# Performance work log

Hardware: AMD Instinct MI355X
Metric: run time of the kernel (lower is better)

## Reference

```python
import jax, jax.numpy as jnp
import numpy as np
from jax import lax

C = 64
EPS = 1e-6

def ln2d(x, w, b):
    # channel-wise LN over HxW per (n, c)
    mean = x.mean(axis=(2, 3), keepdims=True)
    var = ((x - mean) ** 2).mean(axis=(2, 3), keepdims=True)
    return (x - mean) / jnp.sqrt(var + EPS) * w + b

def pw(x, w, b):
    # 1x1 conv: w [O, I], b [O]
    return jnp.einsum('nihw,oi->nohw', x, w) + b[None, :, None, None]

def dwconv3(x, w, b):
    # depthwise 3x3, w [2C, 1, 3, 3]
    y = lax.conv_general_dilated(x, w, window_strides=(1, 1), padding='SAME',
                                 feature_group_count=x.shape[1],
                                 dimension_numbers=('NCHW', 'OIHW', 'NCHW'))
    return y + b[None, :, None, None]

def simple_gate(x):
    x1, x2 = jnp.split(x, 2, axis=1)
    return x1 * x2

def setup_inputs() -> dict:
    key = jax.random.key(0)
    ks = jax.random.split(key, 16)
    s = 0.05
    return {
        'x': jax.random.normal(ks[0], (8, C, 256, 256), jnp.float32),
        'ln1_w': jnp.ones((1, C, 1, 1), jnp.float32),
        'ln1_b': jnp.zeros((1, C, 1, 1), jnp.float32),
        'pw1_w': jax.random.normal(ks[1], (2 * C, C), jnp.float32) * s,
        'pw1_b': jnp.zeros((2 * C,), jnp.float32),
        'dw_w': jax.random.normal(ks[2], (2 * C, 1, 3, 3), jnp.float32) * s,
        'dw_b': jnp.zeros((2 * C,), jnp.float32),
        'sca_w': jax.random.normal(ks[3], (C, C), jnp.float32) * s,
        'sca_b': jnp.zeros((C,), jnp.float32),
        'pw2_w': jax.random.normal(ks[4], (C, C), jnp.float32) * s,
        'pw2_b': jnp.zeros((C,), jnp.float32),
        'ln2_w': jnp.ones((1, C, 1, 1), jnp.float32),
        'ln2_b': jnp.zeros((1, C, 1, 1), jnp.float32),
        'pw3_w': jax.random.normal(ks[5], (2 * C, C), jnp.float32) * s,
        'pw3_b': jnp.zeros((2 * C,), jnp.float32),
        'pw4_w': jax.random.normal(ks[6], (C, C), jnp.float32) * s,
        'pw4_b': jnp.zeros((C,), jnp.float32),
        'beta1': jax.random.normal(ks[7], (1, C, 1, 1), jnp.float32) * 0.1,
        'beta2': jax.random.normal(ks[8], (1, C, 1, 1), jnp.float32) * 0.1,
    }

def reference(x, ln1_w, ln1_b, pw1_w, pw1_b, dw_w, dw_b, sca_w, sca_b,
              pw2_w, pw2_b, ln2_w, ln2_b, pw3_w, pw3_b, pw4_w, pw4_b,
              beta1, beta2):
    y = ln2d(x, ln1_w, ln1_b)
    y = pw(y, pw1_w, pw1_b)
    y = dwconv3(y, dw_w, dw_b)
    y = simple_gate(y)
    # SCA: global avg pool -> 1x1 conv -> sigmoid scale
    s = y.mean(axis=(2, 3), keepdims=True)          # [N, C, 1, 1]
    w = jax.nn.sigmoid(pw(s, sca_w, sca_b))
    y = y * w
    y = pw(y, pw2_w, pw2_b)
    x = x + beta1 * y
    y2 = ln2d(x, ln2_w, ln2_b)
    y2 = pw(y2, pw3_w, pw3_b)
    y2 = simple_gate(y2)
    y2 = pw(y2, pw4_w, pw4_b)
    return x + beta2 * y2
```

## Files before the change

### kernel.cpp

```cpp
#include <hip/hip_runtime.h>
#include <hip/hip_bf16.h>

#define NB 8
#define CC 64
#define HWP 65536

typedef __attribute__((ext_vector_type(8))) short short8;
typedef __attribute__((ext_vector_type(4))) float f32x4;

__device__ __forceinline__ short f2bf(float f) {
  union { float f; unsigned u; } v; v.f = f;
  return (short)((v.u + 0x7FFF + ((v.u >> 16) & 1)) >> 16);
}
__device__ __forceinline__ float bf2f(unsigned short u) {
  union { unsigned u; float f; } v; v.u = ((unsigned)u) << 16; return v.f;
}

__global__ __launch_bounds__(256) void ln_stats_kernel(
    const float* __restrict__ x, const float* __restrict__ lw,
    const float* __restrict__ lb, float* __restrict__ a, float* __restrict__ b) {
  int plane = blockIdx.x;
  int c = plane & 63;
  const float4* p4 = (const float4*)(x + (size_t)plane * HWP);
  float s = 0.f, s2 = 0.f;
  for (int i = threadIdx.x; i < HWP / 4; i += 256) {
    float4 v = p4[i];
    s  += v.x + v.y + v.z + v.w;
    s2 += v.x * v.x + v.y * v.y + v.z * v.z + v.w * v.w;
  }
  for (int off = 32; off; off >>= 1) {
    s  += __shfl_down(s, off);
    s2 += __shfl_down(s2, off);
  }
  __shared__ float ls[4], ls2[4];
  int wid = threadIdx.x >> 6, lid = threadIdx.x & 63;
  if (lid == 0) { ls[wid] = s; ls2[wid] = s2; }
  __syncthreads();
  if (threadIdx.x == 0) {
    float S  = ls[0] + ls[1] + ls[2] + ls[3];
    float S2 = ls2[0] + ls2[1] + ls2[2] + ls2[3];
    float mean = S * (1.f / (float)HWP);
    float var  = S2 * (1.f / (float)HWP) - mean * mean;
    float rstd = rsqrtf(var + 1e-6f);
    float av = rstd * lw[c];
    a[plane] = av;
    b[plane] = lb[c] - mean * av;
  }
}

__global__ void fold_kernel(const float* __restrict__ w, const float* __restrict__ pb,
                            const float* __restrict__ a, const float* __restrict__ b,
                            float* __restrict__ wf, float* __restrict__ cf, int O) {
  int idx = blockIdx.x * blockDim.x + threadIdx.x;
  if (idx >= NB * O) return;
  int n = idx / O, o = idx - n * O;
  const float* an = a + n * 64;
  const float* bn = b + n * 64;
  const float* wo = w + o * 64;
  float* wfo = wf + (size_t)idx * 64;
  float cc = pb[o];
  for (int i = 0; i < 64; i++) { float wv = wo[i]; wfo[i] = wv * an[i]; cc += wv * bn[i]; }
  cf[idx] = cc;
}

__global__ __launch_bounds__(256, 2) void gemm_pw1_kernel(
    const float* __restrict__ x, const float* __restrict__ wf,
    const float* __restrict__ cf, unsigned short* __restrict__ z) {
  int n = blockIdx.y;
  int lane = threadIdx.x & 63, wid = threadIdx.x >> 6;
  int col = lane & 15, quad = lane >> 4;
  short8 a[8][2];
  const float* wfn = wf + (size_t)n * 128 * 64;
  #pragma unroll
  for (int mt = 0; mt < 8; mt++)
    #pragma unroll
    for (int ks = 0; ks < 2; ks++) {
      const float* wp = wfn + (mt * 16 + col) * 64 + ks * 32 + quad * 8;
      short8 v;
      #pragma unroll
      for (int j = 0; j < 8; j++) v[j] = f2bf(wp[j]);
      a[mt][ks] = v;
    }
  float cb[8][4];
  #pragma unroll
  for (int mt = 0; mt < 8; mt++)
    #pragma unroll
    for (int r = 0; r < 4; r++) cb[mt][r] = cf[n * 128 + mt * 16 + quad * 4 + r];
  const float* xn = x + (size_t)n * 64 * HWP;
  unsigned short* zn = z + (size_t)n * 128 * HWP;
  int pxbase = blockIdx.x * 512 + wid * 16 + col;
  for (int tile = 0; tile < 8; tile++) {
    int p = pxbase + tile * 64;
    short8 b[2];
    #pragma unroll
    for (int ks = 0; ks < 2; ks++)
      #pragma unroll
      for (int j = 0; j < 8; j++)
        b[ks][j] = f2bf(xn[(size_t)(ks * 32 + quad * 8 + j) * HWP + p]);
    f32x4 acc[8];
    #pragma unroll
    for (int mt = 0; mt < 8; mt++) {
      acc[mt] = (f32x4){0.f, 0.f, 0.f, 0.f};
      acc[mt] = __builtin_amdgcn_mfma_f32_16x16x32_bf16(a[mt][0], b[0], acc[mt], 0, 0, 0);
      acc[mt] = __builtin_amdgcn_mfma_f32_16x16x32_bf16(a[mt][1], b[1], acc[mt], 0, 0, 0);
    }
    #pragma unroll
    for (int mt = 0; mt < 8; mt++)
      #pragma unroll
      for (int r = 0; r < 4; r++)
        zn[(size_t)(mt * 16 + quad * 4 + r) * HWP + p] =
            (unsigned short)f2bf(acc[mt][r] + cb[mt][r]);
  }
}

__global__ __launch_bounds__(256) void dwgate_kernel(
    const unsigned short* __restrict__ z, const float* __restrict__ dww,
    const float* __restrict__ dwb, unsigned short* __restrict__ t,
    float* __restrict__ pooled2) {
  int blk = blockIdx.x;
  int plane = blk >> 1, half = blk & 1;
  int n = plane >> 6, c = plane & 63;
  int lane = threadIdx.x & 63, wv = threadIdx.x >> 6;
  const unsigned short* z0 = z + ((size_t)n * 128 + c) * HWP;
  const unsigned short* z1 = z0 + (size_t)64 * HWP;
  unsigned short* tp = t + (size_t)plane * HWP;
  float w0[9], w1[9];
  #pragma unroll
  for (int k = 0; k < 9; k++) { w0[k] = dww[c * 9 + k]; w1[k] = dww[(c + 64) * 9 + k]; }
  float bias0 = dwb[c], bias1 = dwb[c + 64];
  int r0 = half * 128 + wv * 32;
  int colb = lane * 4;

  float fa[3][4], la[3], ra[3];
  float fb[3][4], lb_[3], rb[3];

  auto loadrow = [&](const unsigned short* base, int h, float* f, float& l, float& r) {
    if ((unsigned)h < 256u) {
      ushort4 u = *(const ushort4*)(base + h * 256 + colb);
      f[0] = bf2f(u.x); f[1] = bf2f(u.y); f[2] = bf2f(u.z); f[3] = bf2f(u.w);
    } else {
      f[0] = f[1] = f[2] = f[3] = 0.f;
    }
    float ll = __shfl_up(f[3], 1);
    float rr = __shfl_down(f[0], 1);
    l = (lane == 0) ? 0.f : ll;
    r = (lane == 63) ? 0.f : rr;
  };

  loadrow(z0, r0 - 1, fa[0], la[0], ra[0]);
  loadrow(z1, r0 - 1, fb[0], lb_[0], rb[0]);
  loadrow(z0, r0,     fa[1], la[1], ra[1]);
  loadrow(z1, r0,     fb[1], lb_[1], rb[1]);

  float lsum = 0.f;
  #pragma unroll 2
  for (int h = r0; h < r0 + 32; h++) {
    loadrow(z0, h + 1, fa[2], la[2], ra[2]);
    loadrow(z1, h + 1, fb[2], lb_[2], rb[2]);
    float o0[4] = {bias0, bias0, bias0, bias0};
    float o1[4] = {bias1, bias1, bias1, bias1};
    #pragma unroll
    for (int rr_ = 0; rr_ < 3; rr_++) {
      float wl0 = w0[rr_ * 3], wc0 = w0[rr_ * 3 + 1], wr0 = w0[rr_ * 3 + 2];
      float wl1 = w1[rr_ * 3], wc1 = w1[rr_ * 3 + 1], wr1 = w1[rr_ * 3 + 2];
      const float* f0 = fa[rr_]; const float* f1 = fb[rr_];
      float l0 = la[rr_], r0h = ra[rr_], l1 = lb_[rr_], r1h = rb[rr_];
      o0[0] += wl0 * l0    + wc0 * f0[0] + wr0 * f0[1];
      o0[1] += wl0 * f0[0] + wc0 * f0[1] + wr0 * f0[2];
      o0[2] += wl0 * f0[1] + wc0 * f0[2] + wr0 * f0[3];
      o0[3] += wl0 * f0[2] + wc0 * f0[3] + wr0 * r0h;
      o1[0] += wl1 * l1    + wc1 * f1[0] + wr1 * f1[1];
      o1[1] += wl1 * f1[0] + wc1 * f1[1] + wr1 * f1[2];
      o1[2] += wl1 * f1[1] + wc1 * f1[2] + wr1 * f1[3];
      o1[3] += wl1 * f1[2] + wc1 * f1[3] + wr1 * r1h;
    }
    float g0 = o0[0] * o1[0], g1 = o0[1] * o1[1];
    float g2 = o0[2] * o1[2], g3 = o0[3] * o1[3];
    uint2 pk;
    pk.x = (unsigned)(unsigned short)f2bf(g0) | ((unsigned)(unsigned short)f2bf(g1) << 16);
    pk.y = (unsigned)(unsigned short)f2bf(g2) | ((unsigned)(unsigned short)f2bf(g3) << 16);
    *(uint2*)(tp + (size_t)h * 256 + colb) = pk;
    lsum += (g0 + g1) + (g2 + g3);
    #pragma unroll
    for (int i = 0; i < 4; i++) { fa[0][i] = fa[1][i]; fa[1][i] = fa[2][i];
                                  fb[0][i] = fb[1][i]; fb[1][i] = fb[2][i]; }
    la[0] = la[1]; la[1] = la[2]; ra[0] = ra[1]; ra[1] = ra[2];
    lb_[0] = lb_[1]; lb_[1] = lb_[2]; rb[0] = rb[1]; rb[1] = rb[2];
  }
  for (int off = 32; off; off >>= 1) lsum += __shfl_down(lsum, off);
  __shared__ float ls[4];
  if (lane == 0) ls[wv] = lsum;
  __syncthreads();
  if (threadIdx.x == 0) pooled2[plane * 2 + half] = ls[0] + ls[1] + ls[2] + ls[3];
}

__global__ void sca_kernel(const float* __restrict__ pooled2, const float* __restrict__ sw,
                           const float* __restrict__ sb, float* __restrict__ sca) {
  int idx = blockIdx.x * blockDim.x + threadIdx.x;
  if (idx >= 512) return;
  int n = idx >> 6, o = idx & 63;
  float s = sb[o];
  const float* pm = pooled2 + n * 64 * 2;
  for (int i = 0; i < 64; i++)
    s += sw[o * 64 + i] * (pm[i * 2] + pm[i * 2 + 1]) * (1.f / 65536.f);
  sca[idx] = 1.f / (1.f + expf(-s));
}

__global__ void fold_pw2_kernel(const float* __restrict__ w, const float* __restrict__ pb,
                                const float* __restrict__ sca, const float* __restrict__ beta1,
                                float* __restrict__ wf, float* __restrict__ cf) {
  int idx = blockIdx.x * blockDim.x + threadIdx.x;
  if (idx >= 512) return;
  int n = idx >> 6, o = idx & 6 * 10 + 3;
  o = idx & 63;
  float bt = beta1[o];
  const float* sn = sca + n * 64;
  float* wfo = wf + (size_t)idx * 64;
  for (int i = 0; i < 64; i++) wfo[i] = bt * w[o * 64 + i] * sn[i];
  cf[idx] = bt * pb[o];
}

__global__ __launch_bounds__(256, 2) void gemm_pw2_kernel(
    const unsigned short* __restrict__ t, const float* __restrict__ x,
    const float* __restrict__ wf, const float* __restrict__ cf,
    float* __restrict__ x1, float* __restrict__ part_sum, float* __restrict__ part_sq) {
  __shared__ float red_s[4][64], red_q[4][64];
  int n = blockIdx.y;
  int lane = threadIdx.x & 63, wid = threadIdx.x >> 6;
  int col = lane & 15, quad = lane >> 4;
  short8 a[4][2];
  const float* wfn = wf + (size_t)n * 64 * 64;
  #pragma unroll
  for (int mt = 0; mt < 4; mt++)
    #pragma unroll
    for (int ks = 0; ks < 2; ks++) {
      const float* wp = wfn + (mt * 16 + col) * 64 + ks * 32 + quad * 8;
      short8 v;
      #pragma unroll
      for (int j = 0; j < 8; j++) v[j] = f2bf(wp[j]);
      a[mt][ks] = v;
    }
  float cb[4][4];
  #pragma unroll
  for (int mt = 0; mt < 4; mt++)
    #pragma unroll
    for (int r = 0; r < 4; r++) cb[mt][r] = cf[n * 64 + mt * 16 + quad * 4 + r];
  const unsigned short* tn = t + (size_t)n * 64 * HWP;
  const float* xn = x + (size_t)n * 64 * HWP;
  float* x1n = x1 + (size_t)n * 64 * HWP;
  int pxbase = blockIdx.x * 512 + wid * 16 + col;
  float sacc[4][4], qacc[4][4];
  #pragma unroll
  for (int mt = 0; mt < 4; mt++)
    #pragma unroll
    for (int r = 0; r < 4; r++) { sacc[mt][r] = 0.f; qacc[mt][r] = 0.f; }
  for (int tile = 0; tile < 8; tile++) {
    int p = pxbase + tile * 64;
    short8 b[2];
    #pragma unroll
    for (int ks = 0; ks < 2; ks++)
      #pragma unroll
      for (int j = 0; j < 8; j++)
        b[ks][j] = (short)tn[(size_t)(ks * 32 + quad * 8 + j) * HWP + p];
    f32x4 acc[4];
    #pragma unroll
    for (int mt = 0; mt < 4; mt++) {
      acc[mt] = (f32x4){0.f, 0.f, 0.f, 0.f};
      acc[mt] = __builtin_amdgcn_mfma_f32_16x16x32_bf16(a[mt][0], b[0], acc[mt], 0, 0, 0);
      acc[mt] = __builtin_amdgcn_mfma_f32_16x16x32_bf16(a[mt][1], b[1], acc[mt], 0, 0, 0);
    }
    #pragma unroll
    for (int mt = 0; mt < 4; mt++)
      #pragma unroll
      for (int r = 0; r < 4; r++) {
        size_t idx = (size_t)(mt * 16 + quad * 4 + r) * HWP + p;
        float v = xn[idx] + acc[mt][r] + cb[mt][r];
        x1n[idx] = v;
        sacc[mt][r] += v;
        qacc[mt][r] += v * v;
      }
  }
  #pragma unroll
  for (int mt = 0; mt < 4; mt++)
    #pragma unroll
    for (int r = 0; r < 4; r++) {
      float s = sacc[mt][r], q = qacc[mt][r];
      #pragma unroll
      for (int off = 1; off < 16; off <<= 1) {
        s += __shfl_xor(s, off);
        q += __shfl_xor(q, off);
      }
      if (col == 0) {
        int o = mt * 16 + quad * 4 + r;
        red_s[wid][o] = s; red_q[wid][o] = q;
      }
    }
  __syncthreads();
  if (threadIdx.x < 64) {
    int c = threadIdx.x;
    float s = red_s[0][c] + red_s[1][c] + red_s[2][c] + red_s[3][c];
    float q = red_q[0][c] + red_q[1][c] + red_q[2][c] + red_q[3][c];
    size_t pidx = ((size_t)n * 64 + c) * 128 + blockIdx.x;
    part_sum[pidx] = s;
    part_sq[pidx]  = q;
  }
}

__global__ __launch_bounds__(256) void ln2fold_kernel(
    const float* __restrict__ w, const float* __restrict__ pb,
    const float* __restrict__ ps, const float* __restrict__ pq,
    const float* __restrict__ lw, const float* __restrict__ lb,
    float* __restrict__ wf, float* __restrict__ cf) {
  __shared__ float aa[64], bb[64];
  int n = blockIdx.x;
  if (threadIdx.x < 64) {
    int c = threadIdx.x;
    const float* p1 = ps + ((size_t)n * 64 + c) * 128;
    const float* p2 = pq + ((size_t)n * 64 + c) * 128;
    float S = 0.f, S2 = 0.f;
    for (int k = 0; k < 128; k++) { S += p1[k]; S2 += p2[k]; }
    float mean = S * (1.f / (float)HWP);
    float var  = S2 * (1.f / (float)HWP) - mean * mean;
    float rstd = rsqrtf(var + 1e-6f);
    float av = rstd * lw[c];
    aa[c] = av;
    bb[c] = lb[c] - mean * av;
  }
  __syncthreads();
  if (threadIdx.x < 128) {
    int o = threadIdx.x;
    const float* wo = w + o * 64;
    float* wfo = wf + ((size_t)n * 128 + o) * 64;
    float cc = pb[o];
    for (int i = 0; i < 64; i++) { float wv = wo[i]; wfo[i] = wv * aa[i]; cc += wv * bb[i]; }
    cf[n * 128 + o] = cc;
  }
}

__global__ __launch_bounds__(256, 2) void final_mfma_kernel(
    const float* __restrict__ x1, const float* __restrict__ w3f,
    const float* __restrict__ c3f, const float* __restrict__ w4,
    const float* __restrict__ pb4, const float* __restrict__ beta2,
    float* __restrict__ out) {
  __shared__ float s_c3[128];
  __shared__ float s_b2[64];
  __shared__ float s_c4[64];
  __shared__ __align__(16) unsigned g_lds[64 * 33];
  int n = blockIdx.y;
  int lane = threadIdx.x & 63, wid = threadIdx.x >> 6;
  int col = lane & 15, quad = lane >> 4;
  if (threadIdx.x < 128) s_c3[threadIdx.x] = c3f[n * 128 + threadIdx.x];
  if (threadIdx.x < 64) { s_b2[threadIdx.x] = beta2[threadIdx.x]; s_c4[threadIdx.x] = pb4[threadIdx.x]; }
  short8 a3[8][2];
  const float* wfn = w3f + (size_t)n * 128 * 64;
  #pragma unroll
  for (int mt = 0; mt < 8; mt++)
    #pragma unroll
    for (int ks = 0; ks < 2; ks++) {
      const float* wp = wfn + (mt * 16 + col) * 64 + ks * 32 + quad * 8;
      short8 v;
      #pragma unroll
      for (int j = 0; j < 8; j++) v[j] = f2bf(wp[j]);
      a3[mt][ks] = v;
    }
  short8 a4[4][2];
  #pragma unroll
  for (int mt = 0; mt < 4; mt++)
    #pragma unroll
    for (int ks = 0; ks < 2; ks++) {
      const float* wp = w4 + (mt * 16 + col) * 64 + ks * 32 + quad * 8;
      short8 v;
      #pragma unroll
      for (int j = 0; j < 8; j++) v[j] = f2bf(wp[j]);
      a4[mt][ks] = v;
    }
  __syncthreads();
  const float* x1n = x1 + (size_t)n * 64 * HWP;
  float* outn = out + (size_t)n * 64 * HWP;
  int pxbase = blockIdx.x * 512 + wid * 16 + col;
  unsigned* grow = g_lds + (wid * 16 + col) * 33;
  for (int tile = 0; tile < 8; tile++) {
    int p = pxbase + tile * 64;
    short8 b1[2];
    #pragma unroll
    for (int ks = 0; ks < 2; ks++)
      #pragma unroll
      for (int j = 0; j < 8; j++)
        b1[ks][j] = f2bf(x1n[(size_t)(ks * 32 + quad * 8 + j) * HWP + p]);
    f32x4 acc[8];
    #pragma unroll
    for (int mt = 0; mt < 8; mt++) {
      acc[mt] = (f32x4){0.f, 0.f, 0.f, 0.f};
      acc[mt] = __builtin_amdgcn_mfma_f32_16x16x32_bf16(a3[mt][0], b1[0], acc[mt], 0, 0, 0);
      acc[mt] = __builtin_amdgcn_mfma_f32_16x16x32_bf16(a3[mt][1], b1[1], acc[mt], 0, 0, 0);
    }
    #pragma unroll
    for (int mt = 0; mt < 4; mt++)
      #pragma unroll
      for (int rr = 0; rr < 2; rr++) {
        int j0 = mt * 16 + quad * 4 + rr * 2;
        float ga = (acc[mt][rr * 2]     + s_c3[j0])     * (acc[mt + 4][rr * 2]     + s_c3[64 + j0]);
        float gb = (acc[mt][rr * 2 + 1] + s_c3[j0 + 1]) * (acc[mt + 4][rr * 2 + 1] + s_c3[64 + j0 + 1]);
        unsigned lo = (unsigned short)f2bf(ga);
        unsigned hi = (unsigned short)f2bf(gb);
        grow[j0 >> 1] = lo | (hi << 16);
      }
    __syncthreads();
    short8 b2[2];
    #pragma unroll
    for (int ks = 0; ks < 2; ks++)
      #pragma unroll
      for (int w = 0; w < 4; w++) {
        unsigned u = grow[ks * 16 + quad * 4 + w];
        b2[ks][2 * w]     = (short)(u & 0xFFFFu);
        b2[ks][2 * w + 1] = (short)(u >> 16);
      }
    __syncthreads();
    f32x4 acc2[4];
    #pragma unroll
    for (int mt = 0; mt < 4; mt++) {
      acc2[mt] = (f32x4){0.f, 0.f, 0.f, 0.f};
      acc2[mt] = __builtin_amdgcn_mfma_f32_16x16x32_bf16(a4[mt][0], b2[0], acc2[mt], 0, 0, 0);
      acc2[mt] = __builtin_amdgcn_mfma_f32_16x16x32_bf16(a4[mt][1], b2[1], acc2[mt], 0, 0, 0);
    }
    #pragma unroll
    for (int mt = 0; mt < 4; mt++)
      #pragma unroll
      for (int r = 0; r < 4; r++) {
        int o = mt * 16 + quad * 4 + r;
        size_t idx = (size_t)o * HWP + p;
        outn[idx] = x1n[idx] + s_b2[o] * (acc2[mt][r] + s_c4[o]);
      }
  }
}

extern "C" void kernel_launch(void* const* d_in, const int* in_sizes, int n_in,
                              void* d_out, int out_size, void* d_ws, size_t ws_size,
                              hipStream_t stream) {
  const float* x    = (const float*)d_in[0];
  const float* ln1w = (const float*)d_in[1];
  const float* ln1b = (const float*)d_in[2];
  const float* pw1w = (const float*)d_in[3];
  const float* pw1b = (const float*)d_in[4];
  const float* dww  = (const float*)d_in[5];
  const float* dwb  = (const float*)d_in[6];
  const float* scaw = (const float*)d_in[7];
  const float* scab = (const float*)d_in[8];
  const float* pw2w = (const float*)d_in[9];
  const float* pw2b = (const float*)d_in[10];
  const float* ln2w = (const float*)d_in[11];
  const float* ln2b = (const float*)d_in[12];
  const float* pw3w = (const float*)d_in[13];
  const float* pw3b = (const float*)d_in[14];
  const float* pw4w = (const float*)d_in[15];
  const float* pw4b = (const float*)d_in[16];
  const float* beta1= (const float*)d_in[17];
  const float* beta2= (const float*)d_in[18];
  float* out = (float*)d_out;

  char* ws = (char*)d_ws;
  unsigned short* z  = (unsigned short*)ws;
  float*          x1 = (float*)ws;
  unsigned short* t  = (unsigned short*)(ws + 134217728ull);
  float* sm = (float*)(ws + 134217728ull + 67108864ull);
  float* a1 = sm;               float* b1 = a1 + 512;
  float* w1f = b1 + 512;        float* c1f = w1f + 65536;
  float* pooled2 = c1f + 1024;  float* sca = pooled2 + 1024;
  float* w2f = sca + 512;       float* c2f = w2f + 32768;
  float* part_sq = c2f + 512;   float* w3f = part_sq + 65536;
  float* c3f = w3f + 65536;
  float* part_sum = w1f;

  hipLaunchKernelGGL(ln_stats_kernel, dim3(512), dim3(256), 0, stream, x, ln1w, ln1b, a1, b1);
  hipLaunchKernelGGL(fold_kernel, dim3(4), dim3(256), 0, stream, pw1w, pw1b, a1, b1, w1f, c1f, 128);
  hipLaunchKernelGGL(gemm_pw1_kernel, dim3(128, 8), dim3(256), 0, stream, x, w1f, c1f, z);
  hipLaunchKernelGGL(dwgate_kernel, dim3(1024), dim3(256), 0, stream, z, dww, dwb, t, pooled2);
  hipLaunchKernelGGL(sca_kernel, dim3(2), dim3(256), 0, stream, pooled2, scaw, scab, sca);
  hipLaunchKernelGGL(fold_pw2_kernel, dim3(2), dim3(256), 0, stream, pw2w, pw2b, sca, beta1, w2f, c2f);
  hipLaunchKernelGGL(gemm_pw2_kernel, dim3(128, 8), dim3(256), 0, stream, t, x, w2f, c2f, x1,
                     part_sum, part_sq);
  hipLaunchKernelGGL(ln2fold_kernel, dim3(8), dim3(256), 0, stream,
                     pw3w, pw3b, part_sum, part_sq, ln2w, ln2b, w3f, c3f);
  hipLaunchKernelGGL(final_mfma_kernel, dim3(128, 8), dim3(256), 0, stream,
                     x1, w3f, c3f, pw4w, pw4b, beta2, out);
}
```

Baseline: 651.6 us.

## Double-buffer activation loads in pointwise GEMM kernels and double grid size

The three MFMA pointwise-conv kernels now prefetch the next tile's activations (and the residual x in pw2) into registers while the current tile's MFMAs run, with the tile loop fully unrolled. Each block now covers 256 pixels instead of 512, so the grids grow to 256x8 and the LN2 partial-statistics arrays get 256 entries per channel. Those partials move into the output buffer, which is only written by the final kernel. The aim is to hide global-load latency and raise parallelism, at the cost of more registers per thread and possibly lower occupancy.

```diff
diff --git a/kernel.cpp b/kernel.cpp
--- a/kernel.cpp
+++ b/kernel.cpp
@@ -88,21 +88,32 @@
     for (int r = 0; r < 4; r++) cb[mt][r] = cf[n * 128 + mt * 16 + quad * 4 + r];
   const float* xn = x + (size_t)n * 64 * HWP;
   unsigned short* zn = z + (size_t)n * 128 * HWP;
-  int pxbase = blockIdx.x * 512 + wid * 16 + col;
-  for (int tile = 0; tile < 8; tile++) {
+  int pxbase = blockIdx.x * 256 + wid * 16 + col;
+
+  auto load_b = [&](int p, short8* bf) {
+    #pragma unroll
+    for (int ks = 0; ks < 2; ks++) {
+      short8 v;
+      #pragma unroll
+      for (int j = 0; j < 8; j++)
+        v[j] = f2bf(xn[(size_t)(ks * 32 + quad * 8 + j) * HWP + p]);
+      bf[ks] = v;
+    }
+  };
+
+  short8 bb[2][2];
+  load_b(pxbase, bb[0]);
+  #pragma unroll
+  for (int tile = 0; tile < 4; tile++) {
+    int cur = tile & 1, nxt = cur ^ 1;
     int p = pxbase + tile * 64;
-    short8 b[2];
-    #pragma unroll
-    for (int ks = 0; ks < 2; ks++)
-      #pragma unroll
-      for (int j = 0; j < 8; j++)
-        b[ks][j] = f2bf(xn[(size_t)(ks * 32 + quad * 8 + j) * HWP + p]);
+    if (tile < 3) load_b(p + 64, bb[nxt]);
     f32x4 acc[8];
     #pragma unroll
     for (int mt = 0; mt < 8; mt++) {
       acc[mt] = (f32x4){0.f, 0.f, 0.f, 0.f};
-      acc[mt] = __builtin_amdgcn_mfma_f32_16x16x32_bf16(a[mt][0], b[0], acc[mt], 0, 0, 0);
-      acc[mt] = __builtin_amdgcn_mfma_f32_16x16x32_bf16(a[mt][1], b[1], acc[mt], 0, 0, 0);
+      acc[mt] = __builtin_amdgcn_mfma_f32_16x16x32_bf16(a[mt][0], bb[cur][0], acc[mt], 0, 0, 0);
+      acc[mt] = __builtin_amdgcn_mfma_f32_16x16x32_bf16(a[mt][1], bb[cur][1], acc[mt], 0, 0, 0);
     }
     #pragma unroll
     for (int mt = 0; mt < 8; mt++)
@@ -211,8 +222,7 @@
                                 float* __restrict__ wf, float* __restrict__ cf) {
   int idx = blockIdx.x * blockDim.x + threadIdx.x;
   if (idx >= 512) return;
-  int n = idx >> 6, o = idx & 6 * 10 + 3;
-  o = idx & 63;
+  int n = idx >> 6, o = idx & 63;
   float bt = beta1[o];
   const float* sn = sca + n * 64;
   float* wfo = wf + (size_t)idx * 64;
@@ -248,33 +258,54 @@
   const unsigned short* tn = t + (size_t)n * 64 * HWP;
   const float* xn = x + (size_t)n * 64 * HWP;
   float* x1n = x1 + (size_t)n * 64 * HWP;
-  int pxbase = blockIdx.x * 512 + wid * 16 + col;
+  int pxbase = blockIdx.x * 256 + wid * 16 + col;
+
+  auto load_t = [&](int p, short8* bf) {
+    #pragma unroll
+    for (int ks = 0; ks < 2; ks++) {
+      short8 v;
+      #pragma unroll
+      for (int j = 0; j < 8; j++)
+        v[j] = (short)tn[(size_t)(ks * 32 + quad * 8 + j) * HWP + p];
+      bf[ks] = v;
+    }
+  };
+  auto load_x = [&](int p, float (*xv)[4]) {
+    #pragma unroll
+    for (int mt = 0; mt < 4; mt++)
+      #pragma unroll
+      for (int r = 0; r < 4; r++)
+        xv[mt][r] = xn[(size_t)(mt * 16 + quad * 4 + r) * HWP + p];
+  };
+
   float sacc[4][4], qacc[4][4];
   #pragma unroll
   for (int mt = 0; mt < 4; mt++)
     #pragma unroll
     for (int r = 0; r < 4; r++) { sacc[mt][r] = 0.f; qacc[mt][r] = 0.f; }
-  for (int tile = 0; tile < 8; tile++) {
+
+  short8 bb[2][2];
+  float xv[2][4][4];
+  load_t(pxbase, bb[0]);
+  load_x(pxbase, xv[0]);
+  #pragma unroll
+  for (int tile = 0; tile < 4; tile++) {
+    int cur = tile & 1, nxt = cur ^ 1;
     int p = pxbase + tile * 64;
-    short8 b[2];
-    #pragma unroll
-    for (int ks = 0; ks < 2; ks++)
-      #pragma unroll
-      for (int j = 0; j < 8; j++)
-        b[ks][j] = (short)tn[(size_t)(ks * 32 + quad * 8 + j) * HWP + p];
+    if (tile < 3) { load_t(p + 64, bb[nxt]); load_x(p + 64, xv[nxt]); }
     f32x4 acc[4];
     #pragma unroll
     for (int mt = 0; mt < 4; mt++) {
       acc[mt] = (f32x4){0.f, 0.f, 0.f, 0.f};
-      acc[mt] = __builtin_amdgcn_mfma_f32_16x16x32_bf16(a[mt][0], b[0], acc[mt], 0, 0, 0);
-      acc[mt] = __builtin_amdgcn_mfma_f32_16x16x32_bf16(a[mt][1], b[1], acc[mt], 0, 0, 0);
+      acc[mt] = __builtin_amdgcn_mfma_f32_16x16x32_bf16(a[mt][0], bb[cur][0], acc[mt], 0, 0, 0);
+      acc[mt] = __builtin_amdgcn_mfma_f32_16x16x32_bf16(a[mt][1], bb[cur][1], acc[mt], 0, 0, 0);
     }
     #pragma unroll
     for (int mt = 0; mt < 4; mt++)
       #pragma unroll
       for (int r = 0; r < 4; r++) {
         size_t idx = (size_t)(mt * 16 + quad * 4 + r) * HWP + p;
-        float v = xn[idx] + acc[mt][r] + cb[mt][r];
+        float v = xv[cur][mt][r] + acc[mt][r] + cb[mt][r];
         x1n[idx] = v;
         sacc[mt][r] += v;
         qacc[mt][r] += v * v;
@@ -300,7 +331,7 @@
     int c = threadIdx.x;
     float s = red_s[0][c] + red_s[1][c] + red_s[2][c] + red_s[3][c];
     float q = red_q[0][c] + red_q[1][c] + red_q[2][c] + red_q[3][c];
-    size_t pidx = ((size_t)n * 64 + c) * 128 + blockIdx.x;
+    size_t pidx = ((size_t)n * 64 + c) * 256 + blockIdx.x;
     part_sum[pidx] = s;
     part_sq[pidx]  = q;
   }
@@ -315,10 +346,10 @@
   int n = blockIdx.x;
   if (threadIdx.x < 64) {
     int c = threadIdx.x;
-    const float* p1 = ps + ((size_t)n * 64 + c) * 128;
-    const float* p2 = pq + ((size_t)n * 64 + c) * 128;
+    const float* p1 = ps + ((size_t)n * 64 + c) * 256;
+    const float* p2 = pq + ((size_t)n * 64 + c) * 256;
     float S = 0.f, S2 = 0.f;
-    for (int k = 0; k < 128; k++) { S += p1[k]; S2 += p2[k]; }
+    for (int k = 0; k < 256; k++) { S += p1[k]; S2 += p2[k]; }
     float mean = S * (1.f / (float)HWP);
     float var  = S2 * (1.f / (float)HWP) - mean * mean;
     float rstd = rsqrtf(var + 1e-6f);
@@ -377,22 +408,33 @@
   __syncthreads();
   const float* x1n = x1 + (size_t)n * 64 * HWP;
   float* outn = out + (size_t)n * 64 * HWP;
-  int pxbase = blockIdx.x * 512 + wid * 16 + col;
+  int pxbase = blockIdx.x * 256 + wid * 16 + col;
   unsigned* grow = g_lds + (wid * 16 + col) * 33;
-  for (int tile = 0; tile < 8; tile++) {
+
+  auto load_b1 = [&](int p, short8* bf) {
+    #pragma unroll
+    for (int ks = 0; ks < 2; ks++) {
+      short8 v;
+      #pragma unroll
+      for (int j = 0; j < 8; j++)
+        v[j] = f2bf(x1n[(size_t)(ks * 32 + quad * 8 + j) * HWP + p]);
+      bf[ks] = v;
+    }
+  };
+
+  short8 bb1[2][2];
+  load_b1(pxbase, bb1[0]);
+  #pragma unroll
+  for (int tile = 0; tile < 4; tile++) {
+    int cur = tile & 1, nxt = cur ^ 1;
     int p = pxbase + tile * 64;
-    short8 b1[2];
-    #pragma unroll
-    for (int ks = 0; ks < 2; ks++)
-      #pragma unroll
-      for (int j = 0; j < 8; j++)
-        b1[ks][j] = f2bf(x1n[(size_t)(ks * 32 + quad * 8 + j) * HWP + p]);
+    if (tile < 3) load_b1(p + 64, bb1[nxt]);
     f32x4 acc[8];
     #pragma unroll
     for (int mt = 0; mt < 8; mt++) {
       acc[mt] = (f32x4){0.f, 0.f, 0.f, 0.f};
-      acc[mt] = __builtin_amdgcn_mfma_f32_16x16x32_bf16(a3[mt][0], b1[0], acc[mt], 0, 0, 0);
-      acc[mt] = __builtin_amdgcn_mfma_f32_16x16x32_bf16(a3[mt][1], b1[1], acc[mt], 0, 0, 0);
+      acc[mt] = __builtin_amdgcn_mfma_f32_16x16x32_bf16(a3[mt][0], bb1[cur][0], acc[mt], 0, 0, 0);
+      acc[mt] = __builtin_amdgcn_mfma_f32_16x16x32_bf16(a3[mt][1], bb1[cur][1], acc[mt], 0, 0, 0);
     }
     #pragma unroll
     for (int mt = 0; mt < 4; mt++)
@@ -467,20 +509,20 @@
   float* w1f = b1 + 512;        float* c1f = w1f + 65536;
   float* pooled2 = c1f + 1024;  float* sca = pooled2 + 1024;
   float* w2f = sca + 512;       float* c2f = w2f + 32768;
-  float* part_sq = c2f + 512;   float* w3f = part_sq + 65536;
-  float* c3f = w3f + 65536;
-  float* part_sum = w1f;
+  float* w3f = c2f + 512;       float* c3f = w3f + 65536;
+  float* part_sum = (float*)d_out;
+  float* part_sq  = part_sum + 131072;
 
   hipLaunchKernelGGL(ln_stats_kernel, dim3(512), dim3(256), 0, stream, x, ln1w, ln1b, a1, b1);
   hipLaunchKernelGGL(fold_kernel, dim3(4), dim3(256), 0, stream, pw1w, pw1b, a1, b1, w1f, c1f, 128);
-  hipLaunchKernelGGL(gemm_pw1_kernel, dim3(128, 8), dim3(256), 0, stream, x, w1f, c1f, z);
+  hipLaunchKernelGGL(gemm_pw1_kernel, dim3(256, 8), dim3(256), 0, stream, x, w1f, c1f, z);
   hipLaunchKernelGGL(dwgate_kernel, dim3(1024), dim3(256), 0, stream, z, dww, dwb, t, pooled2);
   hipLaunchKernelGGL(sca_kernel, dim3(2), dim3(256), 0, stream, pooled2, scaw, scab, sca);
   hipLaunchKernelGGL(fold_pw2_kernel, dim3(2), dim3(256), 0, stream, pw2w, pw2b, sca, beta1, w2f, c2f);
-  hipLaunchKernelGGL(gemm_pw2_kernel, dim3(128, 8), dim3(256), 0, stream, t, x, w2f, c2f, x1,
+  hipLaunchKernelGGL(gemm_pw2_kernel, dim3(256, 8), dim3(256), 0, stream, t, x, w2f, c2f, x1,
                      part_sum, part_sq);
   hipLaunchKernelGGL(ln2fold_kernel, dim3(8), dim3(256), 0, stream,
                      pw3w, pw3b, part_sum, part_sq, ln2w, ln2b, w3f, c3f);
-  hipLaunchKernelGGL(final_mfma_kernel, dim3(128, 8), dim3(256), 0, stream,
+  hipLaunchKernelGGL(final_mfma_kernel, dim3(256, 8), dim3(256), 0, stream,
                      x1, w3f, c3f, pw4w, pw4b, beta2, out);
 }
```

After: 591.5 us. -9.2%, faster.
